# Kernel optimization log

Measured on AMD Instinct MI355X. Metric: run time of the kernel, lower is better.

Reference implementation:

```python
import jax, jax.numpy as jnp
import numpy as np

C, H, W = 3, 224, 224
P = 14  # patches per row
PS = H // P  # 16
PATCH_DIM = C * PS * PS  # 768
HIDDEN = 768


def patchify(images):
    # images: [n, c, h, w] -> [n, P*P, c*PS*PS], flatten order (c, ph, pw)
    n = images.shape[0]
    x = images.reshape(n, C, P, PS, P, PS)
    x = x.transpose(0, 2, 4, 1, 3, 5)  # [n, Pi, Pj, c, ps, ps]
    return x.reshape(n, P * P, PATCH_DIM)


def setup_inputs() -> dict:
    key = jax.random.key(0)
    k1, k2, k3 = jax.random.split(key, 3)
    images = jax.random.normal(k1, (128, C, H, W), dtype=jnp.float32)
    # nn.Linear(patch_embedding_dim, hidden_dim): weight [out, in], bias [out]
    bound = 1.0 / np.sqrt(PATCH_DIM)
    W_lin = jax.random.uniform(k2, (HIDDEN, PATCH_DIM), minval=-bound, maxval=bound, dtype=jnp.float32)
    b_lin = jax.random.uniform(k3, (HIDDEN,), minval=-bound, maxval=bound, dtype=jnp.float32)
    cls_token = jnp.ones((1, HIDDEN), dtype=jnp.float32)
    return {"images": images, "W_lin": W_lin, "b_lin": b_lin, "cls_token": cls_token}


def reference(images, W_lin, b_lin, cls_token):
    patches = patchify(images)                        # [n, 196, 768]
    hidden = jnp.einsum('npd,hd->nph', patches, W_lin) + b_lin  # [n, 196, H]
    n = images.shape[0]
    cls = jnp.broadcast_to(cls_token[None], (n, 1, HIDDEN))
    return jnp.concatenate([cls, hidden], axis=1)     # [n, 197, H]
```

## Files before the change

kernel.cpp:

```cpp
#include <hip/hip_runtime.h>
#include <cstdint>


#define PGRID 14
#define PSZ   16
#define CHN   3
#define IMGW  224
#define KDIM  768
#define NDIM  768
#define NPATCH 196

typedef short bf16x8 __attribute__((ext_vector_type(8)));
typedef short short8v __attribute__((ext_vector_type(8)));
typedef float f32x4  __attribute__((ext_vector_type(4)));

__device__ __forceinline__ short bf16rne(float f) {
    uint32_t u = __builtin_bit_cast(uint32_t, f);
    u += 0x7FFFu + ((u >> 16) & 1u);
    return (short)(u >> 16);
}

__device__ __forceinline__ short8v cvt8(float4 v0, float4 v1) {
    short8v s;
    s[0] = bf16rne(v0.x); s[1] = bf16rne(v0.y); s[2] = bf16rne(v0.z); s[3] = bf16rne(v0.w);
    s[4] = bf16rne(v1.x); s[5] = bf16rne(v1.y); s[6] = bf16rne(v1.z); s[7] = bf16rne(v1.w);
    return s;
}

__global__ __launch_bounds__(256) void prep_patch(
    const float* __restrict__ img, short* __restrict__ A, int M)
{
    int t = blockIdx.x * 256 + threadIdx.x;
    if (t >= M * 96) return;
    int m  = t / 96;
    int k8 = t - m * 96;
    int k  = k8 * 8;
    int c  = k >> 8;
    int ph = (k >> 4) & 15;
    int pw = k & 15;
    int im = m / NPATCH;
    int p  = m - im * NPATCH;
    int Pi = p / PGRID;
    int Pj = p - Pi * PGRID;
    const float* src = img + (((long)(im * CHN + c) * IMGW + Pi * PSZ + ph) * IMGW + Pj * PSZ + pw);
    float4 v0 = *(const float4*)src;
    float4 v1 = *(const float4*)(src + 4);
    *(short8v*)(A + (long)m * KDIM + k) = cvt8(v0, v1);
}

__global__ __launch_bounds__(256) void prep_small(
    const float* __restrict__ Wl, const float* __restrict__ cls,
    short* __restrict__ Wb, float* __restrict__ out, int n_img)
{
    int t = blockIdx.x * 256 + threadIdx.x;
    const int WCH = KDIM * NDIM / 8;
    if (t < WCH) {
        float4 v0 = *(const float4*)(Wl + (long)t * 8);
        float4 v1 = *(const float4*)(Wl + (long)t * 8 + 4);
        *(short8v*)(Wb + (long)t * 8) = cvt8(v0, v1);
    } else {
        int u = t - WCH;
        if (u < n_img * 96) {
            int im = u / 96;
            int k8 = u - im * 96;
            float4 v0 = *(const float4*)(cls + k8 * 8);
            float4 v1 = *(const float4*)(cls + k8 * 8 + 4);
            float* dst = out + (long)im * 197 * NDIM + k8 * 8;
            *(float4*)dst = v0;
            *(float4*)(dst + 4) = v1;
        }
    }
}

__global__ __launch_bounds__(256) void vit_gemm3(
    const short* __restrict__ A, const short* __restrict__ B,
    const float* __restrict__ bias, float* __restrict__ out,
    int M, int mgroups)
{
    {
    }
    const int bid = blockIdx.x;
    const int xcd = bid & 7;
    const int s   = bid >> 3;
    const int gq  = s / 6;
    const int j   = s - gq * 6;
    const int g   = gq * 8 + xcd;
    if (g >= mgroups) return;
    const int m0 = g * 128;
    const int n0 = j * 128;

    __shared__ short As[128 * 64];
    __shared__ short Bs[128 * 64];

    const int tid = threadIdx.x;
    const int wave = tid >> 6;
    const int lane = tid & 63;

    const int srow = tid >> 3;
    const int sk   = (tid & 7) ^ (srow & 7);
    const long abase = (long)(m0 + srow) * KDIM + sk * 8;
    const long bbase = (long)(n0 + srow) * KDIM + sk * 8;

    const int wm = (wave & 1) * 64;
    const int wn = (wave >> 1) * 64;
    const int wq = lane >> 4;
    const int lr = lane & 15;
    const int blk0 = ((wq)     ^ (lr & 7)) * 8;
    const int blk1 = ((wq + 4) ^ (lr & 7)) * 8;

    f32x4 acc[4][4] = {};
    bf16x8 ra[4], rb[4];

    #pragma unroll
    for (int jj = 0; jj < 4; ++jj) {
        ra[jj] = *(const bf16x8*)(A + abase + (long)jj * 32 * KDIM);
        rb[jj] = *(const bf16x8*)(B + bbase + (long)jj * 32 * KDIM);
    }

    for (int kk = 0; kk < KDIM; kk += 64) {
        #pragma unroll
        for (int jj = 0; jj < 4; ++jj) {
            *(bf16x8*)(&As[(jj * 256 + tid) * 8]) = ra[jj];
            *(bf16x8*)(&Bs[(jj * 256 + tid) * 8]) = rb[jj];
        }
        __syncthreads();

        if (kk + 64 < KDIM) {
            #pragma unroll
            for (int jj = 0; jj < 4; ++jj) {
                ra[jj] = *(const bf16x8*)(A + abase + (long)jj * 32 * KDIM + kk + 64);
                rb[jj] = *(const bf16x8*)(B + bbase + (long)jj * 32 * KDIM + kk + 64);
            }
        }

        #pragma unroll
        for (int ks = 0; ks < 2; ++ks) {
            const int blk = ks ? blk1 : blk0;
            bf16x8 a[4], b[4];
            #pragma unroll
            for (int i = 0; i < 4; ++i)
                a[i] = *(const bf16x8*)(&As[(wm + i * 16 + lr) * 64 + blk]);
            #pragma unroll
            for (int i = 0; i < 4; ++i)
                b[i] = *(const bf16x8*)(&Bs[(wn + i * 16 + lr) * 64 + blk]);
            #pragma unroll
            for (int i = 0; i < 4; ++i)
                #pragma unroll
                for (int jm = 0; jm < 4; ++jm)
                    acc[i][jm] = __builtin_amdgcn_mfma_f32_16x16x32_bf16(a[i], b[jm], acc[i][jm], 0, 0, 0);
        }
        __syncthreads();
    }

    float bv[4];
    #pragma unroll
    for (int jm = 0; jm < 4; ++jm) bv[jm] = bias[n0 + wn + jm * 16 + lr];

    #pragma unroll
    for (int i = 0; i < 4; ++i) {
        #pragma unroll
        for (int r = 0; r < 4; ++r) {
            int gm = m0 + wm + i * 16 + wq * 4 + r;
            if (gm < M) {
                int im = gm / NPATCH;
                int p  = gm - im * NPATCH;
                long orow = ((long)im * 197 + 1 + p) * (long)NDIM;
                #pragma unroll
                for (int jm = 0; jm < 4; ++jm)
                    out[orow + n0 + wn + jm * 16 + lr] = acc[i][jm][r] + bv[jm];
            }
        }
    }
}

#define LDSTR 40
__global__ __launch_bounds__(256) void vit_gemm_fb(
    const float* __restrict__ img, const float* __restrict__ Wl,
    const float* __restrict__ bias, float* __restrict__ out, int n_img)
{
    const int M = n_img * NPATCH;
    __shared__ short As[128 * LDSTR];
    __shared__ short Bs[128 * LDSTR];
    const int tid = threadIdx.x;
    const int m0 = blockIdx.y * 128;
    const int n0 = blockIdx.x * 128;
    const int col4  = tid & 7;
    const int rbase = tid >> 3;
    long arow[4];
    for (int rr = 0; rr < 4; ++rr) {
        int m = m0 + rbase + rr * 32;
        int mm = (m < M) ? m : (M - 1);
        int im = mm / NPATCH;
        int p  = mm % NPATCH;
        int Pi = p / PGRID;
        int Pj = p % PGRID;
        arow[rr] = ((long)(im * CHN) * IMGW + Pi * PSZ) * IMGW + Pj * PSZ;
    }
    const int lane = tid & 63;
    const int wave = tid >> 6;
    const int wm = (wave & 1) * 64;
    const int wn = (wave >> 1) * 64;
    const int wq = lane >> 4;
    const int lr = lane & 15;
    f32x4 acc[4][4] = {};
    for (int k0 = 0; k0 < KDIM; k0 += 32) {
        {
            int k  = k0 + col4 * 4;
            int c  = k >> 8;
            int ph = (k >> 4) & 15;
            int pw = k & 15;
            long koff = (long)(c * IMGW + ph) * IMGW + pw;
            #pragma unroll
            for (int rr = 0; rr < 4; ++rr) {
                const float4 v = *(const float4*)(img + arow[rr] + koff);
                int row = rbase + rr * 32;
                short4 s;
                s.x = bf16rne(v.x); s.y = bf16rne(v.y);
                s.z = bf16rne(v.z); s.w = bf16rne(v.w);
                *(short4*)(&As[row * LDSTR + col4 * 4]) = s;
            }
        }
        {
            int k = k0 + col4 * 4;
            #pragma unroll
            for (int rr = 0; rr < 4; ++rr) {
                int nrow = rbase + rr * 32;
                const float4 v = *(const float4*)(Wl + (long)(n0 + nrow) * KDIM + k);
                short4 s;
                s.x = bf16rne(v.x); s.y = bf16rne(v.y);
                s.z = bf16rne(v.z); s.w = bf16rne(v.w);
                *(short4*)(&Bs[nrow * LDSTR + col4 * 4]) = s;
            }
        }
        __syncthreads();
        bf16x8 a[4], b[4];
        #pragma unroll
        for (int i = 0; i < 4; ++i)
            a[i] = *(const bf16x8*)(&As[(wm + i * 16 + lr) * LDSTR + wq * 8]);
        #pragma unroll
        for (int i = 0; i < 4; ++i)
            b[i] = *(const bf16x8*)(&Bs[(wn + i * 16 + lr) * LDSTR + wq * 8]);
        #pragma unroll
        for (int i = 0; i < 4; ++i)
            #pragma unroll
            for (int j = 0; j < 4; ++j)
                acc[i][j] = __builtin_amdgcn_mfma_f32_16x16x32_bf16(a[i], b[j], acc[i][j], 0, 0, 0);
        __syncthreads();
    }
    float bv[4];
    #pragma unroll
    for (int j = 0; j < 4; ++j) bv[j] = bias[n0 + wn + j * 16 + lr];
    #pragma unroll
    for (int i = 0; i < 4; ++i) {
        #pragma unroll
        for (int r = 0; r < 4; ++r) {
            int gm = m0 + wm + i * 16 + wq * 4 + r;
            if (gm < M) {
                int im = gm / NPATCH;
                int p  = gm % NPATCH;
                long orow = ((long)im * 197 + 1 + p) * (long)NDIM;
                #pragma unroll
                for (int j = 0; j < 4; ++j)
                    out[orow + n0 + wn + j * 16 + lr] = acc[i][j][r] + bv[j];
            }
        }
    }
}

__global__ __launch_bounds__(256) void cls_fill(
    const float* __restrict__ cls, float* __restrict__ out, int n_img)
{
    int i = blockIdx.x * 256 + threadIdx.x;
    if (i < n_img * NDIM) {
        int im = i / NDIM;
        int n  = i - im * NDIM;
        out[(long)im * 197 * NDIM + n] = cls[n];
    }
}

extern "C" void kernel_launch(void* const* d_in, const int* in_sizes, int n_in,
                              void* d_out, int out_size, void* d_ws, size_t ws_size,
                              hipStream_t stream) {
    const float* img  = (const float*)d_in[0];
    const float* Wl   = (const float*)d_in[1];
    const float* bias = (const float*)d_in[2];
    const float* cls  = (const float*)d_in[3];
    float* out = (float*)d_out;

    int n_img = in_sizes[0] / (CHN * IMGW * IMGW);
    int M = n_img * NPATCH;
    int mgroups = (M + 127) / 128;
    long Mpad = (long)mgroups * 128;

    size_t need = (size_t)(Mpad * KDIM + (long)KDIM * NDIM) * sizeof(short);
    if (ws_size >= need) {
        short* A_ws = (short*)d_ws;
        short* Wb   = A_ws + Mpad * KDIM;

        prep_patch<<<(M * 96 + 255) / 256, 256, 0, stream>>>(img, A_ws, M);
        int small_total = KDIM * NDIM / 8 + n_img * 96;
        prep_small<<<(small_total + 255) / 256, 256, 0, stream>>>(Wl, cls, Wb, out, n_img);

        int gpad = (mgroups + 7) & ~7;
        int nblocks = gpad * 6;
        vit_gemm3<<<nblocks, 256, 0, stream>>>(A_ws, Wb, bias, out, M, mgroups);
    } else {
        dim3 grid(NDIM / 128, mgroups);
        vit_gemm_fb<<<grid, 256, 0, stream>>>(img, Wl, bias, out, n_img);
        int cls_elems = n_img * NDIM;
        cls_fill<<<(cls_elems + 255) / 256, 256, 0, stream>>>(cls, out, n_img);
    }
}
```

Before: 179.6 us.

## Fuse patchify and bf16 conversion into the GEMM A-tile loads

After: 196.0 us. 1.09x slower.

```diff
diff --git a/kernel.cpp b/kernel.cpp
--- a/kernel.cpp
+++ b/kernel.cpp
@@ -11,7 +11,6 @@
 #define NPATCH 196
 
 typedef short bf16x8 __attribute__((ext_vector_type(8)));
-typedef short short8v __attribute__((ext_vector_type(8)));
 typedef float f32x4  __attribute__((ext_vector_type(4)));
 
 __device__ __forceinline__ short bf16rne(float f) {
@@ -20,32 +19,23 @@
     return (short)(u >> 16);
 }
 
-__device__ __forceinline__ short8v cvt8(float4 v0, float4 v1) {
-    short8v s;
+__device__ __forceinline__ bf16x8 cvt8(float4 v0, float4 v1) {
+    bf16x8 s;
     s[0] = bf16rne(v0.x); s[1] = bf16rne(v0.y); s[2] = bf16rne(v0.z); s[3] = bf16rne(v0.w);
     s[4] = bf16rne(v1.x); s[5] = bf16rne(v1.y); s[6] = bf16rne(v1.z); s[7] = bf16rne(v1.w);
     return s;
 }
 
-__global__ __launch_bounds__(256) void prep_patch(
-    const float* __restrict__ img, short* __restrict__ A, int M)
-{
-    int t = blockIdx.x * 256 + threadIdx.x;
-    if (t >= M * 96) return;
-    int m  = t / 96;
-    int k8 = t - m * 96;
-    int k  = k8 * 8;
+__device__ __forceinline__ bf16x8 loadA_patch(
+    const float* __restrict__ img, long arowb, int k)
+{
     int c  = k >> 8;
     int ph = (k >> 4) & 15;
     int pw = k & 15;
-    int im = m / NPATCH;
-    int p  = m - im * NPATCH;
-    int Pi = p / PGRID;
-    int Pj = p - Pi * PGRID;
-    const float* src = img + (((long)(im * CHN + c) * IMGW + Pi * PSZ + ph) * IMGW + Pj * PSZ + pw);
+    const float* src = img + arowb + (c * IMGW + ph) * IMGW + pw;
     float4 v0 = *(const float4*)src;
     float4 v1 = *(const float4*)(src + 4);
-    *(short8v*)(A + (long)m * KDIM + k) = cvt8(v0, v1);
+    return cvt8(v0, v1);
 }
 
 __global__ __launch_bounds__(256) void prep_small(
@@ -57,7 +47,7 @@
     if (t < WCH) {
         float4 v0 = *(const float4*)(Wl + (long)t * 8);
         float4 v1 = *(const float4*)(Wl + (long)t * 8 + 4);
-        *(short8v*)(Wb + (long)t * 8) = cvt8(v0, v1);
+        *(bf16x8*)(Wb + (long)t * 8) = cvt8(v0, v1);
     } else {
         int u = t - WCH;
         if (u < n_img * 96) {
@@ -72,13 +62,11 @@
     }
 }
 
-__global__ __launch_bounds__(256) void vit_gemm3(
-    const short* __restrict__ A, const short* __restrict__ B,
+__global__ __launch_bounds__(256) void vit_gemm_fused(
+    const float* __restrict__ img, const short* __restrict__ B,
     const float* __restrict__ bias, float* __restrict__ out,
     int M, int mgroups)
 {
-    {
-    }
     const int bid = blockIdx.x;
     const int xcd = bid & 7;
     const int s   = bid >> 3;
@@ -98,8 +86,20 @@
 
     const int srow = tid >> 3;
     const int sk   = (tid & 7) ^ (srow & 7);
-    const long abase = (long)(m0 + srow) * KDIM + sk * 8;
-    const long bbase = (long)(n0 + srow) * KDIM + sk * 8;
+    const int kbase = sk * 8;
+    const long bbase = (long)(n0 + srow) * KDIM + kbase;
+
+    long arow[4];
+    #pragma unroll
+    for (int jj = 0; jj < 4; ++jj) {
+        int m  = m0 + srow + jj * 32;
+        int mm = (m < M) ? m : (M - 1);
+        int im = mm / NPATCH;
+        int p  = mm - im * NPATCH;
+        int Pi = p / PGRID;
+        int Pj = p - Pi * PGRID;
+        arow[jj] = ((long)(im * CHN) * IMGW + Pi * PSZ) * IMGW + Pj * PSZ;
+    }
 
     const int wm = (wave & 1) * 64;
     const int wn = (wave >> 1) * 64;
@@ -113,7 +113,7 @@
 
     #pragma unroll
     for (int jj = 0; jj < 4; ++jj) {
-        ra[jj] = *(const bf16x8*)(A + abase + (long)jj * 32 * KDIM);
+        ra[jj] = loadA_patch(img, arow[jj], kbase);
         rb[jj] = *(const bf16x8*)(B + bbase + (long)jj * 32 * KDIM);
     }
 
@@ -128,7 +128,7 @@
         if (kk + 64 < KDIM) {
             #pragma unroll
             for (int jj = 0; jj < 4; ++jj) {
-                ra[jj] = *(const bf16x8*)(A + abase + (long)jj * 32 * KDIM + kk + 64);
+                ra[jj] = loadA_patch(img, arow[jj], kk + 64 + kbase);
                 rb[jj] = *(const bf16x8*)(B + bbase + (long)jj * 32 * KDIM + kk + 64);
             }
         }
@@ -290,20 +290,17 @@
     int n_img = in_sizes[0] / (CHN * IMGW * IMGW);
     int M = n_img * NPATCH;
     int mgroups = (M + 127) / 128;
-    long Mpad = (long)mgroups * 128;
-
-    size_t need = (size_t)(Mpad * KDIM + (long)KDIM * NDIM) * sizeof(short);
+
+    size_t need = (size_t)KDIM * NDIM * sizeof(short);
     if (ws_size >= need) {
-        short* A_ws = (short*)d_ws;
-        short* Wb   = A_ws + Mpad * KDIM;
-
-        prep_patch<<<(M * 96 + 255) / 256, 256, 0, stream>>>(img, A_ws, M);
+        short* Wb = (short*)d_ws;
+
         int small_total = KDIM * NDIM / 8 + n_img * 96;
         prep_small<<<(small_total + 255) / 256, 256, 0, stream>>>(Wl, cls, Wb, out, n_img);
 
         int gpad = (mgroups + 7) & ~7;
         int nblocks = gpad * 6;
-        vit_gemm3<<<nblocks, 256, 0, stream>>>(A_ws, Wb, bias, out, M, mgroups);
+        vit_gemm_fused<<<nblocks, 256, 0, stream>>>(img, Wb, bias, out, M, mgroups);
     } else {
         dim3 grid(NDIM / 128, mgroups);
         vit_gemm_fb<<<grid, 256, 0, stream>>>(img, Wl, bias, out, n_img);
```
